# Kernel tuning notes

Measured on AMD Instinct MI355X. Metric: run time of the kernel, lower is better.

The kernel has to match this reference:

```python
import jax, jax.numpy as jnp
import numpy as np

# Module constants (from init_kwargs)
IN_C, OUT_C = 512, 1024
NUM_STEPS, NUM_POINTS = 5, 5
CH_DIMS = 1024          # lcm(512, 1024)
IN_CF = 2               # CH_DIMS // IN_C
OUT_CF = 1              # CH_DIMS // OUT_C
SP_DIMS = 1
BATCH = 16384


def setup_inputs() -> dict:
    key = jax.random.key(0)
    k = jax.random.split(key, 6)
    data = jax.random.normal(k[0], (BATCH, IN_C), dtype=jnp.float32)
    angles = jnp.linspace(0.0, 2.0 * jnp.pi, NUM_POINTS, dtype=jnp.float32).reshape(1, 1, NUM_POINTS)
    velocity = jnp.linspace(0.0, 1.0, NUM_POINTS, dtype=jnp.float32).reshape(1, 1, NUM_POINTS)
    in_weight = jax.random.normal(k[1], (1, CH_DIMS, SP_DIMS), dtype=jnp.float32)
    in_bias = jax.random.normal(k[2], (1, CH_DIMS, SP_DIMS), dtype=jnp.float32)
    out_weight = jax.random.normal(k[3], (1, CH_DIMS, SP_DIMS), dtype=jnp.float32)
    out_bias = jax.random.normal(k[4], (1, CH_DIMS, SP_DIMS), dtype=jnp.float32)
    return {"data": data, "angles": angles, "velocity": velocity,
            "in_weight": in_weight, "in_bias": in_bias,
            "out_weight": out_weight, "out_bias": out_bias}


def _access(mem, idx, bgn, end):
    # mem: (NUM_POINTS,), idx float, bgn/end int of same shape
    pos = idx - bgn.astype(idx.dtype)
    return (1.0 - pos) * mem[bgn] + pos * mem[end]


def _step(d, mem_v, mem_a):
    idx = jax.nn.sigmoid(d) * NUM_POINTS
    bgn = jnp.floor(idx).astype(jnp.int32)
    end = jnp.floor(idx + 1.0).astype(jnp.int32)
    # faithful clamp logic from accessor()
    bgn = jnp.where(bgn + 1 < NUM_POINTS, bgn, bgn - 1) * (bgn >= 0)
    end = (jnp.where(end < NUM_POINTS, end, 0) + jnp.where(end == NUM_POINTS, end - 1, 0)) * (end >= 0)
    velo = _access(mem_v, idx, bgn, end)
    ang = _access(mem_a, idx, bgn, end)
    return velo * jnp.cos(ang) + d * velo * jnp.sin(ang)


def reference(data, angles, velocity, in_weight, in_bias, out_weight, out_bias):
    # expansion: (B, IN_C, 1, 1, 1) * (1, IN_C, IN_CF, 1, 1) + bias -> (B, CH_DIMS, SP_DIMS)
    x = data.reshape(-1, IN_C, 1, SP_DIMS, 1)
    w = in_weight.reshape(1, IN_C, IN_CF, SP_DIMS, 1)
    b = in_bias.reshape(1, IN_C, IN_CF, SP_DIMS, 1)
    x = (x * w + b).reshape(-1, CH_DIMS, SP_DIMS)

    mem_v = velocity.reshape(-1)  # (NUM_POINTS,)
    mem_a = angles.reshape(-1)
    # nonlinear: iterative refinement
    for _ in range(NUM_STEPS):
        x = x + _step(x, mem_v, mem_a) / NUM_STEPS

    # attention + reduction
    att = jax.nn.sigmoid(x * out_weight + out_bias)
    x = x * att
    x = x.reshape(-1, OUT_CF, OUT_C, 1, SP_DIMS)
    return jnp.sum(x, axis=(1, 3))  # (B, OUT_C, SP_DIMS)
```

## Files before the change

### kernel.cpp

```cpp
#include <hip/hip_runtime.h>


constexpr int IN_C  = 512;
constexpr int OUT_C = 1024;

constexpr float LUT_L     = 6.4f;
constexpr float LUT_H     = 0.00625f;
constexpr float LUT_SCALE = 160.0f;
constexpr float LUT_BIAS  = 1024.0f;

typedef float floatx4 __attribute__((ext_vector_type(4)));

__device__ __forceinline__ float fast_sigmoid(float x) {
    float e = __builtin_amdgcn_exp2f(x * -1.44269504088896341f);
    return __builtin_amdgcn_rcpf(1.0f + e);
}

__device__ float exact5(float x) {
    #pragma unroll
    for (int s = 0; s < 5; ++s) {
        const float d    = x;
        const float idx  = 5.0f * fast_sigmoid(d);
        const float velo = idx * 0.25f;
        float rev = idx * 0.25f;
        rev -= (rev >= 1.0f) ? 1.0f : 0.0f;
        const float cs = __builtin_amdgcn_cosf(rev);
        const float sn = __builtin_amdgcn_sinf(rev);
        float step = fmaf(d * velo, sn, velo * cs);
        step = (idx == 5.0f) ? 0.0f : step;
        x = fmaf(step, 0.2f, d);
    }
    return x;
}

__device__ __forceinline__ float tail5(float x) {
    #pragma unroll
    for (int k = 0; k < 5; ++k) {
        const float d  = x;
        const float s  = fast_sigmoid(d);
        const bool  hi = s > 0.5f;
        const float w  = hi ? (1.0f - s) : s;
        const float ph = 7.85398163397448f * w;
        const float c1 = fmaf(-0.5f * ph, ph, 1.0f);
        const float cos_a = hi ? ph : c1;
        const float sin_a = hi ? c1 : ph;
        float step = 1.25f * s * fmaf(d, sin_a, cos_a);
        step = (s == 1.0f) ? 0.0f : step;
        x = fmaf(step, 0.2f, d);
    }
    return x;
}

__global__ __launch_bounds__(1024) void mac_fused(
    const float* __restrict__ data,
    const float* __restrict__ in_w,
    const float* __restrict__ in_b,
    const float* __restrict__ out_w,
    const float* __restrict__ out_b,
    float* __restrict__ out)
{
    __shared__ float lut[2050];

    const int tid = threadIdx.x;
    const int i4  = tid & 127;
    const int r0  = tid >> 7;
    const int b0  = blockIdx.x * 8 + r0;
    const int c0  = i4 * 4;

    const float2 dlo0 = *reinterpret_cast<const float2*>(data + b0 * IN_C + i4 * 2);
    const float2 dhi0 = *reinterpret_cast<const float2*>(data + b0 * IN_C + 256 + i4 * 2);
    const float4 w0  = *reinterpret_cast<const float4*>(in_w + c0);
    const float4 w1  = *reinterpret_cast<const float4*>(in_w + c0 + 512);
    const float4 ib0 = *reinterpret_cast<const float4*>(in_b + c0);
    const float4 ib1 = *reinterpret_cast<const float4*>(in_b + c0 + 512);
    const float4 ow0 = *reinterpret_cast<const float4*>(out_w + c0);
    const float4 ow1 = *reinterpret_cast<const float4*>(out_w + c0 + 512);
    const float4 ob0 = *reinterpret_cast<const float4*>(out_b + c0);
    const float4 ob1 = *reinterpret_cast<const float4*>(out_b + c0 + 512);

    lut[tid]        = exact5(fmaf((float)tid,          LUT_H, -LUT_L));
    lut[tid + 1024] = exact5(fmaf((float)(tid + 1024), LUT_H, -LUT_L));
    if (tid == 1023) {
        const float gtop = exact5(LUT_L);
        lut[2048] = gtop;
        lut[2049] = gtop;
    }

    const float wv[8]  = {w0.x, w0.y, w0.z, w0.w, w1.x, w1.y, w1.z, w1.w};
    const float bv[8]  = {ib0.x, ib0.y, ib0.z, ib0.w, ib1.x, ib1.y, ib1.z, ib1.w};
    const float owv[8] = {ow0.x, ow0.y, ow0.z, ow0.w, ow1.x, ow1.y, ow1.z, ow1.w};
    const float obv[8] = {ob0.x, ob0.y, ob0.z, ob0.w, ob1.x, ob1.y, ob1.z, ob1.w};

    __syncthreads();

    #pragma unroll
    for (int t = 0; t < 4; ++t) {
        const int b = b0 + t * 4096;
        float2 dlo, dhi;
        if (t == 0) { dlo = dlo0; dhi = dhi0; }
        else {
            dlo = *reinterpret_cast<const float2*>(data + b * IN_C + i4 * 2);
            dhi = *reinterpret_cast<const float2*>(data + b * IN_C + 256 + i4 * 2);
        }
        const float din[8] = {dlo.x, dlo.x, dlo.y, dlo.y, dhi.x, dhi.x, dhi.y, dhi.y};

        float xo[8];
        #pragma unroll
        for (int j = 0; j < 8; ++j) {
            const float x0 = fmaf(din[j], wv[j], bv[j]);
            float p = fmaf(x0, LUT_SCALE, LUT_BIAS);
            p = fminf(fmaxf(p, 0.0f), 2048.0f);
            const int   ii = (int)p;
            const float fr = p - (float)ii;
            const float v0 = lut[ii];
            const float v1 = lut[ii + 1];
            float r = fmaf(fr, v1 - v0, v0);
            if (__builtin_expect(__builtin_fabsf(x0) > LUT_L, 0))
                r = tail5(x0);
            const float att = fast_sigmoid(fmaf(r, owv[j], obv[j]));
            xo[j] = r * att;
        }

        const floatx4 o0 = {xo[0], xo[1], xo[2], xo[3]};
        const floatx4 o1 = {xo[4], xo[5], xo[6], xo[7]};
        __builtin_nontemporal_store(o0, reinterpret_cast<floatx4*>(out + b * OUT_C + c0));
        __builtin_nontemporal_store(o1, reinterpret_cast<floatx4*>(out + b * OUT_C + c0 + 512));
    }
}

extern "C" void kernel_launch(void* const* d_in, const int* in_sizes, int n_in,
                              void* d_out, int out_size, void* d_ws, size_t ws_size,
                              hipStream_t stream) {
    const float* data  = (const float*)d_in[0];
    const float* in_w  = (const float*)d_in[3];
    const float* in_b  = (const float*)d_in[4];
    const float* out_w = (const float*)d_in[5];
    const float* out_b = (const float*)d_in[6];
    float* out = (float*)d_out;

    mac_fused<<<512, 1024, 0, stream>>>(data, in_w, in_b, out_w, out_b, out);
}
```

Measured before the change: 22.73 us.

## Halve per-thread channel work and double grid to 1024 blocks

Each thread now handles 4 contiguous output channels for one row instead of 8 split channels, and each block covers 4 rows instead of 8, so the grid doubles to 1024 blocks. Launch bounds add a min-blocks hint of 8 to lower register pressure. This is meant to improve occupancy and latency hiding. In exchange, the per-block LUT precomputation is repeated twice as many times in total.

Result: slower. 25.00 us (+10.0%).

```diff
diff --git a/kernel.cpp b/kernel.cpp
--- a/kernel.cpp
+++ b/kernel.cpp
@@ -51,7 +51,7 @@
     return x;
 }
 
-__global__ __launch_bounds__(1024) void mac_fused(
+__global__ __launch_bounds__(1024, 8) void mac_fused(
     const float* __restrict__ data,
     const float* __restrict__ in_w,
     const float* __restrict__ in_b,
@@ -62,21 +62,16 @@
     __shared__ float lut[2050];
 
     const int tid = threadIdx.x;
-    const int i4  = tid & 127;
-    const int r0  = tid >> 7;
-    const int b0  = blockIdx.x * 8 + r0;
-    const int c0  = i4 * 4;
+    const int q   = tid & 255;
+    const int r0  = tid >> 8;
+    const int b0  = blockIdx.x * 4 + r0;
+    const int c0  = q * 4;
 
-    const float2 dlo0 = *reinterpret_cast<const float2*>(data + b0 * IN_C + i4 * 2);
-    const float2 dhi0 = *reinterpret_cast<const float2*>(data + b0 * IN_C + 256 + i4 * 2);
+    const float2 d0  = *reinterpret_cast<const float2*>(data + b0 * IN_C + q * 2);
     const float4 w0  = *reinterpret_cast<const float4*>(in_w + c0);
-    const float4 w1  = *reinterpret_cast<const float4*>(in_w + c0 + 512);
     const float4 ib0 = *reinterpret_cast<const float4*>(in_b + c0);
-    const float4 ib1 = *reinterpret_cast<const float4*>(in_b + c0 + 512);
     const float4 ow0 = *reinterpret_cast<const float4*>(out_w + c0);
-    const float4 ow1 = *reinterpret_cast<const float4*>(out_w + c0 + 512);
     const float4 ob0 = *reinterpret_cast<const float4*>(out_b + c0);
-    const float4 ob1 = *reinterpret_cast<const float4*>(out_b + c0 + 512);
 
     lut[tid]        = exact5(fmaf((float)tid,          LUT_H, -LUT_L));
     lut[tid + 1024] = exact5(fmaf((float)(tid + 1024), LUT_H, -LUT_L));
@@ -86,27 +81,24 @@
         lut[2049] = gtop;
     }
 
-    const float wv[8]  = {w0.x, w0.y, w0.z, w0.w, w1.x, w1.y, w1.z, w1.w};
-    const float bv[8]  = {ib0.x, ib0.y, ib0.z, ib0.w, ib1.x, ib1.y, ib1.z, ib1.w};
-    const float owv[8] = {ow0.x, ow0.y, ow0.z, ow0.w, ow1.x, ow1.y, ow1.z, ow1.w};
-    const float obv[8] = {ob0.x, ob0.y, ob0.z, ob0.w, ob1.x, ob1.y, ob1.z, ob1.w};
+    const float wv[4]  = {w0.x, w0.y, w0.z, w0.w};
+    const float bv[4]  = {ib0.x, ib0.y, ib0.z, ib0.w};
+    const float owv[4] = {ow0.x, ow0.y, ow0.z, ow0.w};
+    const float obv[4] = {ob0.x, ob0.y, ob0.z, ob0.w};
 
     __syncthreads();
 
     #pragma unroll
     for (int t = 0; t < 4; ++t) {
         const int b = b0 + t * 4096;
-        float2 dlo, dhi;
-        if (t == 0) { dlo = dlo0; dhi = dhi0; }
-        else {
-            dlo = *reinterpret_cast<const float2*>(data + b * IN_C + i4 * 2);
-            dhi = *reinterpret_cast<const float2*>(data + b * IN_C + 256 + i4 * 2);
-        }
-        const float din[8] = {dlo.x, dlo.x, dlo.y, dlo.y, dhi.x, dhi.x, dhi.y, dhi.y};
+        float2 dl;
+        if (t == 0) dl = d0;
+        else        dl = *reinterpret_cast<const float2*>(data + b * IN_C + q * 2);
+        const float din[4] = {dl.x, dl.x, dl.y, dl.y};
 
-        float xo[8];
+        float xo[4];
         #pragma unroll
-        for (int j = 0; j < 8; ++j) {
+        for (int j = 0; j < 4; ++j) {
             const float x0 = fmaf(din[j], wv[j], bv[j]);
             float p = fmaf(x0, LUT_SCALE, LUT_BIAS);
             p = fminf(fmaxf(p, 0.0f), 2048.0f);
@@ -121,10 +113,8 @@
             xo[j] = r * att;
         }
 
-        const floatx4 o0 = {xo[0], xo[1], xo[2], xo[3]};
-        const floatx4 o1 = {xo[4], xo[5], xo[6], xo[7]};
-        __builtin_nontemporal_store(o0, reinterpret_cast<floatx4*>(out + b * OUT_C + c0));
-        __builtin_nontemporal_store(o1, reinterpret_cast<floatx4*>(out + b * OUT_C + c0 + 512));
+        const floatx4 o = {xo[0], xo[1], xo[2], xo[3]};
+        __builtin_nontemporal_store(o, reinterpret_cast<floatx4*>(out + b * OUT_C + c0));
     }
 }
 
@@ -138,5 +128,5 @@
     const float* out_b = (const float*)d_in[6];
     float* out = (float*)d_out;
 
-    mac_fused<<<512, 1024, 0, stream>>>(data, in_w, in_b, out_w, out_b, out);
+    mac_fused<<<1024, 1024, 0, stream>>>(data, in_w, in_b, out_w, out_b, out);
 }
```

## Pair LUT entries as float2 and give each thread contiguous channels

Applied to the files above, without the earlier changes.

The lookup table is rebuilt into a float2 array of adjacent node pairs, so each interpolation needs one 64-bit LDS read instead of two scalar reads. The thread-to-channel mapping also changes: each thread now owns 8 contiguous output channels and reads a float4 of input, replacing the two split halves 512 apart. This cuts the number of LDS and global load instructions. In exchange it adds an extra barrier, a second LUT build pass and more shared memory, and the output stores now have a stride of 32 bytes between lanes.

Measured after the change: 27.65 us. 21.7% more time.

```diff
diff --git a/kernel.cpp b/kernel.cpp
--- a/kernel.cpp
+++ b/kernel.cpp
@@ -59,32 +59,36 @@
     const float* __restrict__ out_b,
     float* __restrict__ out)
 {
-    __shared__ float lut[2050];
+    __shared__ float  nodes[2050];
+    __shared__ float2 lut2[2049];
 
     const int tid = threadIdx.x;
     const int i4  = tid & 127;
     const int r0  = tid >> 7;
     const int b0  = blockIdx.x * 8 + r0;
-    const int c0  = i4 * 4;
+    const int c0  = i4 * 8;
 
-    const float2 dlo0 = *reinterpret_cast<const float2*>(data + b0 * IN_C + i4 * 2);
-    const float2 dhi0 = *reinterpret_cast<const float2*>(data + b0 * IN_C + 256 + i4 * 2);
+    const float4 d40 = *reinterpret_cast<const float4*>(data + b0 * IN_C + i4 * 4);
     const float4 w0  = *reinterpret_cast<const float4*>(in_w + c0);
-    const float4 w1  = *reinterpret_cast<const float4*>(in_w + c0 + 512);
+    const float4 w1  = *reinterpret_cast<const float4*>(in_w + c0 + 4);
     const float4 ib0 = *reinterpret_cast<const float4*>(in_b + c0);
-    const float4 ib1 = *reinterpret_cast<const float4*>(in_b + c0 + 512);
+    const float4 ib1 = *reinterpret_cast<const float4*>(in_b + c0 + 4);
     const float4 ow0 = *reinterpret_cast<const float4*>(out_w + c0);
-    const float4 ow1 = *reinterpret_cast<const float4*>(out_w + c0 + 512);
+    const float4 ow1 = *reinterpret_cast<const float4*>(out_w + c0 + 4);
     const float4 ob0 = *reinterpret_cast<const float4*>(out_b + c0);
-    const float4 ob1 = *reinterpret_cast<const float4*>(out_b + c0 + 512);
+    const float4 ob1 = *reinterpret_cast<const float4*>(out_b + c0 + 4);
 
-    lut[tid]        = exact5(fmaf((float)tid,          LUT_H, -LUT_L));
-    lut[tid + 1024] = exact5(fmaf((float)(tid + 1024), LUT_H, -LUT_L));
+    nodes[tid]        = exact5(fmaf((float)tid,          LUT_H, -LUT_L));
+    nodes[tid + 1024] = exact5(fmaf((float)(tid + 1024), LUT_H, -LUT_L));
     if (tid == 1023) {
         const float gtop = exact5(LUT_L);
-        lut[2048] = gtop;
-        lut[2049] = gtop;
+        nodes[2048] = gtop;
+        nodes[2049] = gtop;
     }
+    __syncthreads();
+    lut2[tid]        = make_float2(nodes[tid],        nodes[tid + 1]);
+    lut2[tid + 1024] = make_float2(nodes[tid + 1024], nodes[tid + 1025]);
+    if (tid == 1023) lut2[2048] = make_float2(nodes[2048], nodes[2049]);
 
     const float wv[8]  = {w0.x, w0.y, w0.z, w0.w, w1.x, w1.y, w1.z, w1.w};
     const float bv[8]  = {ib0.x, ib0.y, ib0.z, ib0.w, ib1.x, ib1.y, ib1.z, ib1.w};
@@ -96,13 +100,10 @@
     #pragma unroll
     for (int t = 0; t < 4; ++t) {
         const int b = b0 + t * 4096;
-        float2 dlo, dhi;
-        if (t == 0) { dlo = dlo0; dhi = dhi0; }
-        else {
-            dlo = *reinterpret_cast<const float2*>(data + b * IN_C + i4 * 2);
-            dhi = *reinterpret_cast<const float2*>(data + b * IN_C + 256 + i4 * 2);
-        }
-        const float din[8] = {dlo.x, dlo.x, dlo.y, dlo.y, dhi.x, dhi.x, dhi.y, dhi.y};
+        float4 d4;
+        if (t == 0) d4 = d40;
+        else        d4 = *reinterpret_cast<const float4*>(data + b * IN_C + i4 * 4);
+        const float din[8] = {d4.x, d4.x, d4.y, d4.y, d4.z, d4.z, d4.w, d4.w};
 
         float xo[8];
         #pragma unroll
@@ -112,9 +113,8 @@
             p = fminf(fmaxf(p, 0.0f), 2048.0f);
             const int   ii = (int)p;
             const float fr = p - (float)ii;
-            const float v0 = lut[ii];
-            const float v1 = lut[ii + 1];
-            float r = fmaf(fr, v1 - v0, v0);
+            const float2 pr = lut2[ii];
+            float r = fmaf(fr, pr.y - pr.x, pr.x);
             if (__builtin_expect(__builtin_fabsf(x0) > LUT_L, 0))
                 r = tail5(x0);
             const float att = fast_sigmoid(fmaf(r, owv[j], obv[j]));
@@ -124,7 +124,7 @@
         const floatx4 o0 = {xo[0], xo[1], xo[2], xo[3]};
         const floatx4 o1 = {xo[4], xo[5], xo[6], xo[7]};
         __builtin_nontemporal_store(o0, reinterpret_cast<floatx4*>(out + b * OUT_C + c0));
-        __builtin_nontemporal_store(o1, reinterpret_cast<floatx4*>(out + b * OUT_C + c0 + 512));
+        __builtin_nontemporal_store(o1, reinterpret_cast<floatx4*>(out + b * OUT_C + c0 + 4));
     }
 }
 
```
